# Kernel optimization log

Measured on AMD Instinct MI355X. Metric: run time of the kernel, lower is better.

## Reference

```python
import jax, jax.numpy as jnp
import numpy as np

H = 12          # num attention heads
D = 768         # hidden size
DH = D // H     # head dim = 64

def setup_inputs() -> dict:
    key = jax.random.key(0)
    ks = jax.random.split(key, 9)
    B, N = 8, 1024
    s = 0.02
    return {
        "hidden_states": jax.random.normal(ks[0], (B, N, D), jnp.float32),
        "Wq": jax.random.normal(ks[1], (D, D), jnp.float32) * s,
        "bq": jnp.zeros((D,), jnp.float32),
        "Wk": jax.random.normal(ks[2], (D, D), jnp.float32) * s,
        "bk": jnp.zeros((D,), jnp.float32),
        "Wv": jax.random.normal(ks[3], (D, D), jnp.float32) * s,
        "bv": jnp.zeros((D,), jnp.float32),
        "Wo": jax.random.normal(ks[4], (D, D), jnp.float32) * s,
        "bo": jnp.zeros((D,), jnp.float32),
    }

def _split_heads(x):
    # [B, N, D] -> [B, H, N, DH]
    B, N, _ = x.shape
    return x.reshape(B, N, H, DH).transpose(0, 2, 1, 3)

def reference(hidden_states, Wq, bq, Wk, bk, Wv, bv, Wo, bo):
    # torch Linear: y = x @ W.T + b
    q = _split_heads(hidden_states @ Wq.T + bq)
    k = _split_heads(hidden_states @ Wk.T + bk)
    v = _split_heads(hidden_states @ Wv.T + bv)
    scale = 1.0 / jnp.sqrt(jnp.asarray(DH, hidden_states.dtype))
    scores = jnp.einsum("bhqd,bhkd->bhqk", q, k) * scale
    probs = jax.nn.softmax(scores, axis=-1)
    ctx = jnp.einsum("bhqk,bhkd->bhqd", probs, v)
    B, _, N, _ = ctx.shape
    ctx = ctx.transpose(0, 2, 1, 3).reshape(B, N, D)
    return ctx @ Wo.T + bo
```

## Files before the change

kernel.cpp:

```cpp
#include <hip/hip_runtime.h>

typedef unsigned short u16;
typedef unsigned int   u32;
typedef unsigned long long u64;
typedef __attribute__((ext_vector_type(8))) short bf16x8;
typedef __attribute__((ext_vector_type(4))) float f32x4;
typedef __attribute__((address_space(3))) u32 lds_u32;
typedef __attribute__((address_space(1))) u32 gbl_u32;

#define MFMA16(a,b,c) __builtin_amdgcn_mfma_f32_16x16x32_bf16((a),(b),(c),0,0,0)
#define QSCALE 0.1803368801111204f

#define WAIT3 do{ asm volatile("s_waitcnt vmcnt(3)" ::: "memory"); }while(0)
#define WAIT2 do{ asm volatile("s_waitcnt vmcnt(2)" ::: "memory"); }while(0)
#define WAIT4 do{ asm volatile("s_waitcnt vmcnt(4)" ::: "memory"); }while(0)
#define WAIT0 do{ asm volatile("s_waitcnt vmcnt(0)" ::: "memory"); }while(0)
#define SCHED __builtin_amdgcn_sched_barrier(0)
#define BARR  __builtin_amdgcn_s_barrier()

__device__ __forceinline__ u16 f2bf(float f){
  u32 u = __builtin_bit_cast(u32, f);
  u32 r = u + 0x7fffu + ((u>>16)&1u);
  return (u16)(r>>16);
}
__device__ __forceinline__ float bf2f(u16 h){
  return __builtin_bit_cast(float, (u32)h<<16);
}

union V8 { u16 s[8]; uint4 v; };

__global__ __launch_bounds__(256) void cvt_all(const float* __restrict__ hs,
    const float* __restrict__ Wq, const float* __restrict__ Wk,
    const float* __restrict__ Wv, const float* __restrict__ Wo,
    u16* __restrict__ hsb, u16* __restrict__ wqkv, u16* __restrict__ woh)
{
  const int bid = blockIdx.x;
  if (bid < 3072){
    int i = bid*256 + threadIdx.x;
    const float4* p = (const float4*)(hs + (size_t)i*8);
    float4 a = p[0], b = p[1];
    V8 t;
    t.s[0]=f2bf(a.x); t.s[1]=f2bf(a.y); t.s[2]=f2bf(a.z); t.s[3]=f2bf(a.w);
    t.s[4]=f2bf(b.x); t.s[5]=f2bf(b.y); t.s[6]=f2bf(b.z); t.s[7]=f2bf(b.w);
    *(uint4*)(hsb + (size_t)i*8) = t.v;
    return;
  }
  const int r = bid - 3072;
  const int seg = r / 288;
  const int off = (r - seg*288)*256 + threadIdx.x;
  const float* src = seg==0?Wq: seg==1?Wk: seg==2?Wv: Wo;
  const float4* p = (const float4*)(src + (size_t)off*8);
  float4 a = p[0], b = p[1];
  float xs[8] = {a.x,a.y,a.z,a.w,b.x,b.y,b.z,b.w};
  V8 t;
  #pragma unroll
  for (int j=0;j<8;++j) t.s[j]=f2bf(xs[j]);
  if (seg < 3) *(uint4*)(wqkv + (size_t)seg*589824 + (size_t)off*8) = t.v;
  else         *(uint4*)(woh  + (size_t)off*8) = t.v;
}

__global__ __launch_bounds__(512) void mm_qkv(const u16* __restrict__ A, const u16* __restrict__ Bp,
    const float* __restrict__ bq, const float* __restrict__ bk, const float* __restrict__ bvv,
    u16* __restrict__ Oq, u16* __restrict__ Ok, u16* __restrict__ Ov)
{
  __shared__ u16 P[3][10240];
  const int bid = blockIdx.x;
  const int sid = (bid & 7)*96 + (bid >> 3);
  const int mb = sid/12, nb = sid - mb*12;
  const int m0 = mb*128, n0 = nb*192;
  const int tid = threadIdx.x;
  const int lane = tid&63, wid = tid>>6;
  const int wm = wid>>2, wn = wid&3;
  const int fr = lane&15, fg = lane>>4;
  const int nst = (wid<4) ? 3 : 2;

  const char* Ab = (const char*)A;
  const char* Bb = (const char*)Bp;
  const char* sp[3];
  int ldst[3];
  #pragma unroll
  for (int c=0;c<3;++c){
    int ci = c*512 + tid;
    if (c==2) ci = 1024 + tid;
    if (ci < 512){
      int line = ci>>3, slot = ci&7;
      int d = slot ^ (line&7);
      int row = 2*line + (d>>2);
      sp[c] = Ab + (size_t)(m0+row)*1536 + (d&3)*16;
    } else if (ci < 1280){
      int i = ci - 512;
      int line = i>>3, slot = i&7;
      int d = slot ^ (line&7);
      int row = 2*line + (d>>2);
      sp[c] = Bb + (size_t)(n0+row)*1536 + (d&3)*16;
    } else {
      sp[c] = Ab;
    }
    ldst[c] = ci*16;
  }

  const int sl = (((fr&1)<<2) + fg) ^ (fr>>1);
  const int aoff = (fr&~1)*64 + sl*16 + wm*4096;
  const int boff = 8192 + (fr&~1)*64 + sl*16 + wn*3072;

  f32x4 zz = {0.f,0.f,0.f,0.f};
  f32x4 acc[4][3];
  #pragma unroll
  for (int i=0;i<4;++i)
    #pragma unroll
    for (int j=0;j<3;++j) acc[i][j]=zz;

  auto STAGE = [&](int t, int b){
    char* dst0 = (char*)P[b];
    #pragma unroll
    for (int c=0;c<3;++c){
      if (c==2 && wid>=4) break;
      __builtin_amdgcn_global_load_lds((const gbl_u32*)(sp[c] + (size_t)t*64),
        (lds_u32*)(dst0 + ldst[c]), 16, 0, 0);
    }
  };
  auto COMPUTE = [&](int b){
    const char* pb = (const char*)P[b];
    bf16x8 bfr[3];
    #pragma unroll
    for (int nt=0;nt<3;++nt)
      bfr[nt] = *(const bf16x8*)(pb + boff + nt*1024);
    #pragma unroll
    for (int mt=0;mt<4;++mt){
      bf16x8 af = *(const bf16x8*)(pb + aoff + mt*1024);
      #pragma unroll
      for (int nt=0;nt<3;++nt)
        acc[mt][nt] = MFMA16(af, bfr[nt], acc[mt][nt]);
    }
  };

  STAGE(0, 0); STAGE(1, 1);
  int cb = 0;
  for (int t=0; t<24; ++t){
    if (t < 23){ if (wid < 4) WAIT3; else WAIT2; } else WAIT0;
    BARR; SCHED;
    if (t < 22){
      int sb = cb + 2; if (sb >= 3) sb -= 3;
      STAGE(t+2, sb);
    }
    __builtin_amdgcn_s_setprio(1);
    COMPUTE(cb);
    __builtin_amdgcn_s_setprio(0);
    cb = (cb == 2) ? 0 : cb + 1;
  }

  const int seg = nb/4;
  const float* bias = seg==0?bq: seg==1?bk:bvv;
  const float sc = (seg==0) ? QSCALE : 1.0f;
  if (seg < 2){
    u16* O = seg==0?Oq:Ok;
    #pragma unroll
    for (int mt=0;mt<4;++mt){
      #pragma unroll
      for (int nt=0;nt<3;++nt){
        int colw = n0 + wn*48 + nt*16 + fr - seg*768;
        float bz = bias[colw];
        int hh = colw>>6, d = colw&63;
        #pragma unroll
        for (int rr=0;rr<4;++rr){
          int row = m0 + wm*64 + mt*16 + fg*4 + rr;
          int b = row>>10, nn = row&1023;
          O[((size_t)(b*12+hh)<<16) + (size_t)nn*64 + d] = f2bf((acc[mt][nt][rr] + bz) * sc);
        }
      }
    }
  } else {
    #pragma unroll
    for (int mt=0;mt<4;++mt){
      #pragma unroll
      for (int nt=0;nt<3;++nt){
        int colw = n0 + wn*48 + nt*16 + fr - 1536;
        float bz = bias[colw];
        int hh = colw>>6, d = colw&63;
        int row0 = m0 + wm*64 + mt*16 + fg*4;
        int b = row0>>10, nn = row0&1023;
        union { u16 h[4]; u64 q; } pk;
        #pragma unroll
        for (int rr=0;rr<4;++rr) pk.h[rr] = f2bf(acc[mt][nt][rr] + bz);
        *(u64*)&Ov[((size_t)(b*12+hh)<<16) + (size_t)d*1024 + nn] = pk.q;
      }
    }
  }
}

__global__ __launch_bounds__(256) void mm_o(const u16* __restrict__ A, const u16* __restrict__ Bp,
                                            const float* __restrict__ bias, float* __restrict__ O)
{
  __shared__ u16 P[3][8192];
  const int bid = blockIdx.x;
  const int sid = (bid & 7)*48 + (bid >> 3);
  const int mb = sid/6, nb = sid - mb*6;
  const int m0 = mb*128, n0 = nb*128;
  const int tid = threadIdx.x;
  const int lane = tid&63, wid = tid>>6;
  const int wr = wid>>1, wc = wid&1;
  const int fr = lane&15, fg = lane>>4;

  const char* Ab = (const char*)A;
  const char* Bb = (const char*)Bp;
  const char* sp[4];
  #pragma unroll
  for (int c=0;c<4;++c){
    int ci = c*256 + tid;
    int row = ci>>3, slot = ci&7;
    int d = slot ^ (row&7);
    if (d < 4) sp[c] = Ab + (size_t)(m0+row)*1536 + d*16;
    else       sp[c] = Bb + (size_t)(n0+row)*1536 + (d-4)*16;
  }
  const int sA = (fg ^ (fr&7)) << 4;
  const int sB = sA ^ 64;

  f32x4 zz = {0.f,0.f,0.f,0.f};
  f32x4 acc[4][4];
  #pragma unroll
  for (int i=0;i<4;++i)
    #pragma unroll
    for (int j=0;j<4;++j) acc[i][j]=zz;

  auto STAGE = [&](int t, int b){
    char* dst0 = (char*)P[b];
    #pragma unroll
    for (int c=0;c<4;++c)
      __builtin_amdgcn_global_load_lds((const gbl_u32*)(sp[c] + (size_t)t*64),
        (lds_u32*)(dst0 + c*4096 + wid*1024), 16, 0, 0);
  };
  auto COMPUTE = [&](int b){
    const char* pb = (const char*)P[b];
    bf16x8 bfr[4];
    #pragma unroll
    for (int nt=0;nt<4;++nt)
      bfr[nt] = *(const bf16x8*)(pb + (wc*64+nt*16+fr)*128 + sB);
    #pragma unroll
    for (int mt=0;mt<4;++mt){
      bf16x8 af = *(const bf16x8*)(pb + (wr*64+mt*16+fr)*128 + sA);
      #pragma unroll
      for (int nt=0;nt<4;++nt)
        acc[mt][nt] = MFMA16(af, bfr[nt], acc[mt][nt]);
    }
  };

  STAGE(0, 0); STAGE(1, 1);
  int cb = 0;
  for (int t=0; t<24; ++t){
    if (t < 23) WAIT4; else WAIT0;
    BARR; SCHED;
    if (t < 22){
      int sb = cb + 2; if (sb >= 3) sb -= 3;
      STAGE(t+2, sb);
    }
    __builtin_amdgcn_s_setprio(1);
    COMPUTE(cb);
    __builtin_amdgcn_s_setprio(0);
    cb = (cb == 2) ? 0 : cb + 1;
  }

  #pragma unroll
  for (int mt=0;mt<4;++mt){
    #pragma unroll
    for (int nt=0;nt<4;++nt){
      int colb = n0 + wc*64 + nt*16 + fr;
      float bz = bias[colb];
      #pragma unroll
      for (int rr=0;rr<4;++rr){
        int row = m0 + wr*64 + mt*16 + fg*4 + rr;
        O[(size_t)row*768 + colb] = acc[mt][nt][rr] + bz;
      }
    }
  }
}

__global__ __launch_bounds__(256, 2) void attn(const u16* __restrict__ qh, const u16* __restrict__ kh,
                                               const u16* __restrict__ vh, u16* __restrict__ ch)
{
  __shared__ u16 Kb[2][4096];
  __shared__ u16 Vb[2][4096];
  __shared__ u16 Ps[4][64][72];
  const int tid=threadIdx.x, w=tid>>6, lane=tid&63;
  const int fr=lane&15, fg=lane>>4;
  const int bh=blockIdx.x, qt=blockIdx.y;
  const size_t base=(size_t)bh<<16;
  const int q0=qt*256 + w*64;

  const char* kbase = (const char*)(kh + base);
  const char* vbase = (const char*)(vh + base);

  int koff[2], voff[2];
  #pragma unroll
  for (int c=0;c<2;++c){
    int ci = c*256 + tid;
    int row = ci>>3;
    int colp = ((ci&7)*16) ^ ((row&7)<<4);
    koff[c] = row*128  + colp;
    voff[c] = row*2048 + colp;
  }

  bf16x8 qf[4][2];
  #pragma unroll
  for (int mt=0;mt<4;++mt)
    #pragma unroll
    for (int ks=0;ks<2;++ks)
      qf[mt][ks] = *(const bf16x8*)&qh[base + (size_t)(q0+mt*16+fr)*64 + ks*32 + fg*8];

  const int swz = (fr&7)<<4;
  int lowD[2];
  #pragma unroll
  for (int ks=0;ks<2;++ks) lowD[ks] = (ks*64 + fg*16) ^ swz;
  const int frbase = fr*128;

  const short one_bf = (short)0x3F80;
  bf16x8 ones = {one_bf,one_bf,one_bf,one_bf,one_bf,one_bf,one_bf,one_bf};

  f32x4 zz = {0.f,0.f,0.f,0.f};
  f32x4 o[4][4];
  f32x4 ol[4];
  #pragma unroll
  for (int mt=0;mt<4;++mt){
    ol[mt]=zz;
    #pragma unroll
    for (int j=0;j<4;++j) o[mt][j]=zz;
  }

  {
    #pragma unroll
    for (int c=0;c<2;++c){
      __builtin_amdgcn_global_load_lds((const gbl_u32*)(kbase + koff[c]),
        (lds_u32*)((char*)&Kb[0][0] + c*4096 + w*1024), 16, 0, 0);
      __builtin_amdgcn_global_load_lds((const gbl_u32*)(vbase + voff[c]),
        (lds_u32*)((char*)&Vb[0][0] + c*4096 + w*1024), 16, 0, 0);
    }
  }
  __syncthreads();

  for (int kt=0; kt<16; ++kt){
    const int buf = kt & 1;
    {
      const int ktn = (kt+1) & 15;
      const char* kt_ = kbase + ktn*8192;
      const char* vt_ = vbase + ktn*128;
      #pragma unroll
      for (int c=0;c<2;++c){
        __builtin_amdgcn_global_load_lds((const gbl_u32*)(kt_ + koff[c]),
          (lds_u32*)((char*)&Kb[buf^1][0] + c*4096 + w*1024), 16, 0, 0);
        __builtin_amdgcn_global_load_lds((const gbl_u32*)(vt_ + voff[c]),
          (lds_u32*)((char*)&Vb[buf^1][0] + c*4096 + w*1024), 16, 0, 0);
      }
    }

    f32x4 s[4][4];
    #pragma unroll
    for (int mt=0;mt<4;++mt)
      #pragma unroll
      for (int j=0;j<4;++j) s[mt][j]=zz;
    const char* kb = (const char*)&Kb[buf][0];
    __builtin_amdgcn_s_setprio(1);
    #pragma unroll
    for (int ct=0;ct<4;++ct){
      #pragma unroll
      for (int ks=0;ks<2;++ks){
        bf16x8 kf = *(const bf16x8*)(kb + ct*2048 + frbase + lowD[ks]);
        #pragma unroll
        for (int mt=0;mt<4;++mt)
          s[mt][ct]=MFMA16(kf,qf[mt][ks],s[mt][ct]);
      }
    }
    __builtin_amdgcn_s_setprio(0);

    #pragma unroll
    for (int mt=0;mt<4;++mt){
      #pragma unroll
      for (int ct=0;ct<4;++ct){
        float e0 = __builtin_amdgcn_exp2f(s[mt][ct][0]);
        float e1 = __builtin_amdgcn_exp2f(s[mt][ct][1]);
        float e2 = __builtin_amdgcn_exp2f(s[mt][ct][2]);
        float e3 = __builtin_amdgcn_exp2f(s[mt][ct][3]);
        u32 w0, w1;
        asm("v_cvt_pk_bf16_f32 %0, %1, %2" : "=v"(w0) : "v"(e0), "v"(e1));
        asm("v_cvt_pk_bf16_f32 %0, %1, %2" : "=v"(w1) : "v"(e2), "v"(e3));
        uint2 pk2; pk2.x = w0; pk2.y = w1;
        *(uint2*)&Ps[w][mt*16+fr][ct*16+fg*4] = pk2;
      }
    }

    const char* vb = (const char*)&Vb[buf][0];
    __builtin_amdgcn_s_setprio(1);
    #pragma unroll
    for (int ks2=0;ks2<2;++ks2){
      bf16x8 vf[4];
      #pragma unroll
      for (int dt=0;dt<4;++dt)
        vf[dt] = *(const bf16x8*)(vb + dt*2048 + frbase + lowD[ks2]);
      #pragma unroll
      for (int mt=0;mt<4;++mt){
        bf16x8 pa = *(const bf16x8*)&Ps[w][mt*16+fr][ks2*32+fg*8];
        #pragma unroll
        for (int dt=0;dt<4;++dt)
          o[mt][dt]=MFMA16(pa, vf[dt], o[mt][dt]);
        ol[mt]=MFMA16(pa, ones, ol[mt]);
      }
    }
    __builtin_amdgcn_s_setprio(0);

    __syncthreads();
  }

  const int b=bh/12, hd=bh%12;
  #pragma unroll
  for (int mt=0;mt<4;++mt){
    float inv[4];
    #pragma unroll
    for (int rr=0;rr<4;++rr) inv[rr] = 1.0f / ol[mt][rr];
    #pragma unroll
    for (int dt=0;dt<4;++dt){
      int d = dt*16 + fr;
      #pragma unroll
      for (int rr=0;rr<4;++rr){
        int n = q0 + mt*16 + fg*4 + rr;
        ch[((size_t)b*1024 + n)*768 + hd*64 + d] = f2bf(o[mt][dt][rr] * inv[rr]);
      }
    }
  }
}

extern "C" void kernel_launch(void* const* d_in, const int* in_sizes, int n_in,
                              void* d_out, int out_size, void* d_ws, size_t ws_size,
                              hipStream_t stream) {
  const float* hs = (const float*)d_in[0];
  const float* Wq = (const float*)d_in[1];
  const float* bq = (const float*)d_in[2];
  const float* Wk = (const float*)d_in[3];
  const float* bk = (const float*)d_in[4];
  const float* Wv = (const float*)d_in[5];
  const float* bv = (const float*)d_in[6];
  const float* Wo = (const float*)d_in[7];
  const float* bo = (const float*)d_in[8];
  float* out = (float*)d_out;

  const size_t PS = (size_t)8192*768;
  u16* ws16  = (u16*)d_ws;
  u16* hs_bf = ws16;
  u16* q_bf  = ws16 + PS;
  u16* k_bf  = ws16 + 2*PS;
  u16* v_bf  = ws16 + 3*PS;
  u16* wqkv  = ws16 + 4*PS;
  u16* woh   = wqkv + 3*589824;
  u16* c_hi  = hs_bf;

  dim3 blk(256);
  cvt_all<<<3072 + 4*288, blk, 0, stream>>>(hs, Wq, Wk, Wv, Wo, hs_bf, wqkv, woh);
  mm_qkv<<<768, dim3(512), 0, stream>>>(hs_bf, wqkv, bq, bk, bv, q_bf, k_bf, v_bf);
  attn<<<dim3(96,4), blk, 0, stream>>>(q_bf, k_bf, v_bf, c_hi);
  mm_o<<<384, blk, 0, stream>>>(c_hi, woh, bo, out);
}
```

Measured before the change: 110.4 us.

## Retile output projection GEMM to 128x192 tiles with 512-thread blocks

The output projection GEMM moves from 128x128 tiles on 256 threads to 128x192 tiles on 512 threads (8 waves as 2x4, each computing 64x48). It reuses the mm_qkv staging layout, where A and B rows are interleaved in pairs with an XOR swizzle and the last load chunk goes only to waves 0-3. Wait counts are adjusted per wave. Fewer, larger blocks (256 instead of 384) give more reuse per loaded tile and a better fit to the 256-CU count, at the cost of more LDS per block.

```diff
diff --git a/kernel.cpp b/kernel.cpp
--- a/kernel.cpp
+++ b/kernel.cpp
@@ -13,7 +13,6 @@
 
 #define WAIT3 do{ asm volatile("s_waitcnt vmcnt(3)" ::: "memory"); }while(0)
 #define WAIT2 do{ asm volatile("s_waitcnt vmcnt(2)" ::: "memory"); }while(0)
-#define WAIT4 do{ asm volatile("s_waitcnt vmcnt(4)" ::: "memory"); }while(0)
 #define WAIT0 do{ asm volatile("s_waitcnt vmcnt(0)" ::: "memory"); }while(0)
 #define SCHED __builtin_amdgcn_sched_barrier(0)
 #define BARR  __builtin_amdgcn_s_barrier()
@@ -72,7 +71,6 @@
   const int lane = tid&63, wid = tid>>6;
   const int wm = wid>>2, wn = wid&3;
   const int fr = lane&15, fg = lane>>4;
-  const int nst = (wid<4) ? 3 : 2;
 
   const char* Ab = (const char*)A;
   const char* Bb = (const char*)Bp;
@@ -188,58 +186,75 @@
   }
 }
 
-__global__ __launch_bounds__(256) void mm_o(const u16* __restrict__ A, const u16* __restrict__ Bp,
+__global__ __launch_bounds__(512) void mm_o(const u16* __restrict__ A, const u16* __restrict__ Bp,
                                             const float* __restrict__ bias, float* __restrict__ O)
 {
-  __shared__ u16 P[3][8192];
+  __shared__ u16 P[3][10240];
   const int bid = blockIdx.x;
-  const int sid = (bid & 7)*48 + (bid >> 3);
-  const int mb = sid/6, nb = sid - mb*6;
-  const int m0 = mb*128, n0 = nb*128;
+  const int sid = (bid & 7)*32 + (bid >> 3);
+  const int mb = sid/4, nb = sid & 3;
+  const int m0 = mb*128, n0 = nb*192;
   const int tid = threadIdx.x;
   const int lane = tid&63, wid = tid>>6;
-  const int wr = wid>>1, wc = wid&1;
+  const int wm = wid>>2, wn = wid&3;
   const int fr = lane&15, fg = lane>>4;
 
   const char* Ab = (const char*)A;
   const char* Bb = (const char*)Bp;
-  const char* sp[4];
-  #pragma unroll
-  for (int c=0;c<4;++c){
-    int ci = c*256 + tid;
-    int row = ci>>3, slot = ci&7;
-    int d = slot ^ (row&7);
-    if (d < 4) sp[c] = Ab + (size_t)(m0+row)*1536 + d*16;
-    else       sp[c] = Bb + (size_t)(n0+row)*1536 + (d-4)*16;
-  }
-  const int sA = (fg ^ (fr&7)) << 4;
-  const int sB = sA ^ 64;
+  const char* sp[3];
+  int ldst[3];
+  #pragma unroll
+  for (int c=0;c<3;++c){
+    int ci = c*512 + tid;
+    if (c==2) ci = 1024 + tid;
+    if (ci < 512){
+      int line = ci>>3, slot = ci&7;
+      int d = slot ^ (line&7);
+      int row = 2*line + (d>>2);
+      sp[c] = Ab + (size_t)(m0+row)*1536 + (d&3)*16;
+    } else if (ci < 1280){
+      int i = ci - 512;
+      int line = i>>3, slot = i&7;
+      int d = slot ^ (line&7);
+      int row = 2*line + (d>>2);
+      sp[c] = Bb + (size_t)(n0+row)*1536 + (d&3)*16;
+    } else {
+      sp[c] = Ab;
+    }
+    ldst[c] = ci*16;
+  }
+
+  const int sl = (((fr&1)<<2) + fg) ^ (fr>>1);
+  const int aoff = (fr&~1)*64 + sl*16 + wm*4096;
+  const int boff = 8192 + (fr&~1)*64 + sl*16 + wn*3072;
 
   f32x4 zz = {0.f,0.f,0.f,0.f};
-  f32x4 acc[4][4];
+  f32x4 acc[4][3];
   #pragma unroll
   for (int i=0;i<4;++i)
     #pragma unroll
-    for (int j=0;j<4;++j) acc[i][j]=zz;
+    for (int j=0;j<3;++j) acc[i][j]=zz;
 
   auto STAGE = [&](int t, int b){
     char* dst0 = (char*)P[b];
     #pragma unroll
-    for (int c=0;c<4;++c)
+    for (int c=0;c<3;++c){
+      if (c==2 && wid>=4) break;
       __builtin_amdgcn_global_load_lds((const gbl_u32*)(sp[c] + (size_t)t*64),
-        (lds_u32*)(dst0 + c*4096 + wid*1024), 16, 0, 0);
+        (lds_u32*)(dst0 + ldst[c]), 16, 0, 0);
+    }
   };
   auto COMPUTE = [&](int b){
     const char* pb = (const char*)P[b];
-    bf16x8 bfr[4];
-    #pragma unroll
-    for (int nt=0;nt<4;++nt)
-      bfr[nt] = *(const bf16x8*)(pb + (wc*64+nt*16+fr)*128 + sB);
+    bf16x8 bfr[3];
+    #pragma unroll
+    for (int nt=0;nt<3;++nt)
+      bfr[nt] = *(const bf16x8*)(pb + boff + nt*1024);
     #pragma unroll
     for (int mt=0;mt<4;++mt){
-      bf16x8 af = *(const bf16x8*)(pb + (wr*64+mt*16+fr)*128 + sA);
-      #pragma unroll
-      for (int nt=0;nt<4;++nt)
+      bf16x8 af = *(const bf16x8*)(pb + aoff + mt*1024);
+      #pragma unroll
+      for (int nt=0;nt<3;++nt)
         acc[mt][nt] = MFMA16(af, bfr[nt], acc[mt][nt]);
     }
   };
@@ -247,7 +262,7 @@
   STAGE(0, 0); STAGE(1, 1);
   int cb = 0;
   for (int t=0; t<24; ++t){
-    if (t < 23) WAIT4; else WAIT0;
+    if (t < 23){ if (wid < 4) WAIT3; else WAIT2; } else WAIT0;
     BARR; SCHED;
     if (t < 22){
       int sb = cb + 2; if (sb >= 3) sb -= 3;
@@ -262,12 +277,12 @@
   #pragma unroll
   for (int mt=0;mt<4;++mt){
     #pragma unroll
-    for (int nt=0;nt<4;++nt){
-      int colb = n0 + wc*64 + nt*16 + fr;
+    for (int nt=0;nt<3;++nt){
+      int colb = n0 + wn*48 + nt*16 + fr;
       float bz = bias[colb];
       #pragma unroll
       for (int rr=0;rr<4;++rr){
-        int row = m0 + wr*64 + mt*16 + fg*4 + rr;
+        int row = m0 + wm*64 + mt*16 + fg*4 + rr;
         O[(size_t)row*768 + colb] = acc[mt][nt][rr] + bz;
       }
     }
@@ -454,5 +469,5 @@
   cvt_all<<<3072 + 4*288, blk, 0, stream>>>(hs, Wq, Wk, Wv, Wo, hs_bf, wqkv, woh);
   mm_qkv<<<768, dim3(512), 0, stream>>>(hs_bf, wqkv, bq, bk, bv, q_bf, k_bf, v_bf);
   attn<<<dim3(96,4), blk, 0, stream>>>(q_bf, k_bf, v_bf, c_hi);
-  mm_o<<<384, blk, 0, stream>>>(c_hi, woh, bo, out);
-}
+  mm_o<<<256, dim3(512), 0, stream>>>(c_hi, woh, bo, out);
+}
```

After: 108.9 us. Within noise of the previous version (-1.4%).
